# Kernel optimization log

Measured on AMD Instinct MI355X. Metric: run time of the kernel, lower is better.

## Reference

```python
import jax, jax.numpy as jnp
import numpy as np

NUM_HEADS = 16
LN_EPS = 1e-5


def _transpose_qkv(X, num_heads):
    # Faithful to the repo's (buggy) transpose_qkv:
    # (B,S,D) -> (B,S,H,D/H) -> permute (B,H,S,D/H) -> reshape (B,S,D)
    B, S, D = X.shape
    X = X.reshape(B, S, num_heads, D // num_heads)
    X = jnp.transpose(X, (0, 2, 1, 3))
    return X.reshape(B, S, D)


def _layer_norm(x, w, b):
    mu = jnp.mean(x, axis=-1, keepdims=True)
    var = jnp.var(x, axis=-1, keepdims=True)
    return (x - mu) * jax.lax.rsqrt(var + LN_EPS) * w + b


def setup_inputs() -> dict:
    key = jax.random.key(0)
    ks = jax.random.split(key, 4)
    B, S, D = 4, 2048, 1024
    scale = 1.0 / np.sqrt(D)
    return {
        "src": jax.random.normal(ks[0], (B, S, D), dtype=jnp.float32),
        "W_q": jax.random.normal(ks[1], (D, D), dtype=jnp.float32) * scale,
        "W_k": jax.random.normal(ks[2], (D, D), dtype=jnp.float32) * scale,
        "W_v": jax.random.normal(ks[3], (D, D), dtype=jnp.float32) * scale,
        "ln1_w": jnp.ones((D,), dtype=jnp.float32),
        "ln1_b": jnp.zeros((D,), dtype=jnp.float32),
        "ln2_w": jnp.ones((D,), dtype=jnp.float32),
        "ln2_b": jnp.zeros((D,), dtype=jnp.float32),
    }


def reference(src, W_q, W_k, W_v, ln1_w, ln1_b, ln2_w, ln2_b):
    # W_* stored as (in, out): y = x @ W  (equivalent to torch Linear, bias=False)
    q = _transpose_qkv(src @ W_q, NUM_HEADS)  # (B,S,D)
    k = _transpose_qkv(src @ W_k, NUM_HEADS)
    v = _transpose_qkv(src @ W_v, NUM_HEADS)
    d = q.shape[-1]  # note: full hidden dim, per the buggy transpose_qkv
    scores = jnp.einsum("bqd,bkd->bqk", q, k) / jnp.sqrt(jnp.float32(d))
    a = jax.nn.softmax(scores, axis=-1)          # (B,S,S) attention weights
    att = jnp.einsum("bqk,bkd->bqd", a, v)       # (B,S,D)
    src2 = _layer_norm(att, ln1_w, ln1_b)        # norm1
    X = _layer_norm(src + src2, ln2_w, ln2_b)    # AddNorm (dropout=0 in eval)
    return (X, a)
```

## Files before the change

### kernel.cpp

```cpp
#include <hip/hip_runtime.h>

typedef _Float16 f16;
typedef __attribute__((ext_vector_type(2))) _Float16 f16x2;
typedef __attribute__((ext_vector_type(4))) _Float16 f16x4;
typedef __attribute__((ext_vector_type(8))) _Float16 f16x8;
typedef __attribute__((ext_vector_type(4))) float f32x4;

#define D_MODEL 1024
#define SEQ 2048
#define NBATCH 4
#define NROWS (NBATCH * SEQ)

__device__ __forceinline__ void gload16(const void* g, void* l) {
  __builtin_amdgcn_global_load_lds(
      (__attribute__((address_space(1))) void*)(void*)g,
      (__attribute__((address_space(3))) void*)l, 16, 0, 0);
}

#define BARF                                   \
  do {                                         \
    asm volatile("" ::: "memory");             \
    __builtin_amdgcn_s_barrier();              \
    asm volatile("" ::: "memory");             \
  } while (0)
#define LGK asm volatile("s_waitcnt lgkmcnt(0)" ::: "memory")
#define PRIO1 __builtin_amdgcn_s_setprio(1)
#define PRIO0 __builtin_amdgcn_s_setprio(0)


#define STAGE_A(D, H)                                        \
  {                                                          \
    f16* d_ = lds + ((D) * 2 + (H)) * 8192 + t * 8;          \
    gload16((H) ? aP2 : aP0, d_);                            \
    gload16((H) ? aP3 : aP1, d_ + 4096);                     \
  }
#define STAGE_B(D, H)                                        \
  {                                                          \
    if constexpr (BN == 256) {                               \
      f16* d_ = lds + 32768 + ((D) * 2 + (H)) * 8192 + t * 8;\
      gload16((H) ? bP2 : bP0, d_);                          \
      gload16((H) ? bP3 : bP1, d_ + 4096);                   \
    } else {                                                 \
      f16* d_ = lds + 32768 + (D) * 8192 + t * 8;            \
      gload16(bP0, d_);                                      \
      gload16(bP1, d_ + 4096);                               \
    }                                                        \
  }
#define ADVA                                                 \
  {                                                          \
    if (ka < NT - 1) {                                       \
      ka++;                                                  \
      aP0 += stepA; aP1 += stepA; aP2 += stepA; aP3 += stepA;\
    }                                                        \
  }
#define ADVB                                                 \
  {                                                          \
    if (kb < NT - 1) {                                       \
      kb++;                                                  \
      bP0 += stepB; bP1 += stepB;                            \
      if constexpr (BN == 256) { bP2 += stepB; bP3 += stepB; } \
    }                                                        \
  }
#define VMC_STEADY                                           \
  {                                                          \
    if constexpr (BN == 256) {                               \
      asm volatile("s_waitcnt vmcnt(4)" ::: "memory");       \
    } else {                                                 \
      asm volatile("s_waitcnt vmcnt(2)" ::: "memory");       \
    }                                                        \
  }
#define RD_A(D, MH)                                          \
  _Pragma("unroll") for (int mi = 0; mi < 4; ++mi)           \
  _Pragma("unroll") for (int kh = 0; kh < 2; ++kh) {         \
    const int rr = (MH) * 64 + mi * 16 + fr;                 \
    fa[mi][kh] = *(const f16x8*)(lds + ((D) * 2 + wm) * 8192 \
        + rr * 64 + (((g0 + kh * 4) ^ (rr & 7)) << 3));      \
  }
#define RD_B(D, NH)                                          \
  _Pragma("unroll") for (int j = 0; j < NJ; ++j)             \
  _Pragma("unroll") for (int kh = 0; kh < 2; ++kh) {         \
    int rbr, base;                                           \
    if constexpr (BN == 256) {                               \
      rbr = (wn & 1) * 64 + fr * 4 + (NH) * 2 + j;           \
      base = 32768 + ((D) * 2 + (wn >> 1)) * 8192;           \
    } else {                                                 \
      rbr = wn * 32 + fr * 2 + (NH);                         \
      base = 32768 + (D) * 8192;                             \
    }                                                        \
    fb[NH][j][kh] = *(const f16x8*)(lds + base + rbr * 64 +  \
        (((g0 + kh * 4) ^ ((rbr >> 2) & 7)) << 3));          \
  }
#define MFMA_Q(MH, NH)                                       \
  _Pragma("unroll") for (int mi = 0; mi < 4; ++mi)           \
  _Pragma("unroll") for (int j = 0; j < NJ; ++j)             \
  _Pragma("unroll") for (int kh = 0; kh < 2; ++kh)           \
    acc[((MH) * 4 + mi) * 2 * NJ + (NH) * NJ + j] =          \
        __builtin_amdgcn_mfma_f32_16x16x32_f16(              \
            fa[mi][kh], fb[NH][j][kh],                       \
            acc[((MH) * 4 + mi) * 2 * NJ + (NH) * NJ + j], 0, 0, 0);

template <int BN>
__device__ __forceinline__ void gemm8p(
    const f16* aP0, const f16* aP1, const f16* aP2, const f16* aP3,
    const f16* bP0, const f16* bP1, const f16* bP2, const f16* bP3,
    int stepA, int stepB, int NT, f16* lds, f32x4* acc)
{
  constexpr int NJ = BN / 128;
  const int t = threadIdx.x, l = t & 63;
  const int w = t >> 6, wm = w >> 2, wn = w & 3;
  const int fr = l & 15, g0 = l >> 4;
  f16x8 fa[4][2], fb[2][NJ][2];
#pragma unroll
  for (int i = 0; i < 8 * 2 * NJ; ++i) acc[i] = f32x4{0.f, 0.f, 0.f, 0.f};
  int ka = 0, kb = 0;
  (void)bP2; (void)bP3;

  STAGE_A(0, 0); STAGE_A(0, 1); ADVA;
  if constexpr (BN == 256) { STAGE_B(0, 0); STAGE_B(0, 1); }
  else { STAGE_B(0, 0); }
  ADVB;
  if constexpr (BN == 256) { STAGE_B(1, 0); STAGE_B(1, 1); }
  else { STAGE_B(1, 0); }
  ADVB;
  VMC_STEADY;
  BARF;

#pragma unroll 1
  for (int it = 0; it < NT / 2; ++it) {
    RD_A(0, 0); RD_B(0, 0);
    STAGE_A(1, 0);
    BARF; LGK;
    PRIO1; MFMA_Q(0, 0); PRIO0;
    BARF;
    RD_B(0, 1);
    STAGE_A(1, 1); ADVA;
    BARF; LGK;
    PRIO1; MFMA_Q(0, 1); PRIO0;
    BARF;
    RD_A(0, 1);
    STAGE_B(0, 0);
    if constexpr (BN == 128) ADVB;
    BARF; LGK;
    PRIO1; MFMA_Q(1, 0); PRIO0;
    BARF;
    if constexpr (BN == 256) { STAGE_B(0, 1); ADVB; }
    VMC_STEADY;
    BARF;
    PRIO1; MFMA_Q(1, 1); PRIO0;
    BARF;
    RD_A(1, 0); RD_B(1, 0);
    STAGE_A(0, 0);
    BARF; LGK;
    PRIO1; MFMA_Q(0, 0); PRIO0;
    BARF;
    RD_B(1, 1);
    STAGE_A(0, 1); ADVA;
    BARF; LGK;
    PRIO1; MFMA_Q(0, 1); PRIO0;
    BARF;
    RD_A(1, 1);
    STAGE_B(1, 0);
    if constexpr (BN == 128) ADVB;
    BARF; LGK;
    PRIO1; MFMA_Q(1, 0); PRIO0;
    BARF;
    if constexpr (BN == 256) { STAGE_B(1, 1); ADVB; }
    VMC_STEADY;
    BARF;
    PRIO1; MFMA_Q(1, 1); PRIO0;
    BARF;
  }
}

__global__ __launch_bounds__(512, 2) void k_qkv3(
    const f16* __restrict__ srch, const f16* __restrict__ wt,
    f16* __restrict__ qp, f16* __restrict__ kp, f16* __restrict__ vp)
{
  __shared__ f16 lds[49152];
  const int t = threadIdx.x, l = t & 63;
  const int w = t >> 6, wm = w >> 2, wn = w & 3;
  const int fr = l & 15, g0 = l >> 4, c = t & 7;
  const int z = blockIdx.y >> 3, cb = blockIdx.y & 7;
  const f16 *aP[4], *bP[2];
#pragma unroll
  for (int i = 0; i < 4; ++i) {
    const int rl = i * 64 + (t >> 3);
    aP[i] = srch + (size_t)(blockIdx.x * 256 + rl) * 1024 + ((c ^ (rl & 7)) << 3);
  }
#pragma unroll
  for (int i = 0; i < 2; ++i) {
    const int rl = i * 64 + (t >> 3);
    bP[i] = wt + ((size_t)z << 20) + (size_t)(cb * 128 + rl) * 1024 +
            ((c ^ ((rl >> 2) & 7)) << 3);
  }
  f32x4 acc[16];
  gemm8p<128>(aP[0], aP[1], aP[2], aP[3], bP[0], bP[1], bP[0], bP[0],
              64, 64, 16, lds, acc);
  f16* dst = (z == 0) ? qp : (z == 1 ? kp : vp);
  const int col = cb * 128 + wn * 32 + fr * 2;
#pragma unroll
  for (int mi = 0; mi < 8; ++mi)
#pragma unroll
    for (int q = 0; q < 4; ++q) {
      const int row = blockIdx.x * 256 + wm * 128 + mi * 16 + g0 * 4 + q;
      f16x2 o = {(f16)acc[mi * 2 + 0][q], (f16)acc[mi * 2 + 1][q]};
      *(f16x2*)(dst + (size_t)row * 1024 + col) = o;
    }
}

__global__ __launch_bounds__(512, 2) void k_scores(
    const f16* __restrict__ qp, const f16* __restrict__ kp,
    f16* __restrict__ abf)
{
  __shared__ f16 lds[65536];
  const int t = threadIdx.x, l = t & 63;
  const int w = t >> 6, wm = w >> 2, wn = w & 3;
  const int fr = l & 15, g0 = l >> 4, c = t & 7;
  const int b = blockIdx.z;
  const f16* qb = qp + ((size_t)b << 21);
  const f16* kb = kp + ((size_t)b << 21);
  const f16 *aP[4], *bP[4];
#pragma unroll
  for (int i = 0; i < 4; ++i) {
    const int rl = i * 64 + (t >> 3);
    const int spA = blockIdx.x * 256 + rl;
    aP[i] = qb + (size_t)((spA & 127) << 4) * 1024 + ((spA >> 7) << 6) +
            ((c ^ (rl & 7)) << 3);
    const int spB = blockIdx.y * 256 + rl;
    bP[i] = kb + (size_t)((spB & 127) << 4) * 1024 + ((spB >> 7) << 6) +
            ((c ^ ((rl >> 2) & 7)) << 3);
  }
  f32x4 acc[32];
  gemm8p<256>(aP[0], aP[1], aP[2], aP[3], bP[0], bP[1], bP[2], bP[3],
              1024, 1024, 16, lds, acc);
  f16* Cb = abf + ((size_t)b << 22);
  const int col = blockIdx.y * 256 + wn * 64 + fr * 4;
#pragma unroll
  for (int mi = 0; mi < 8; ++mi)
#pragma unroll
    for (int q = 0; q < 4; ++q) {
      const int row = blockIdx.x * 256 + wm * 128 + mi * 16 + g0 * 4 + q;
      f16x4 o = {(f16)(acc[mi * 4 + 0][q] * 0.03125f),
                 (f16)(acc[mi * 4 + 1][q] * 0.03125f),
                 (f16)(acc[mi * 4 + 2][q] * 0.03125f),
                 (f16)(acc[mi * 4 + 3][q] * 0.03125f)};
      *(f16x4*)(Cb + (size_t)row * 2048 + col) = o;
    }
}

__global__ __launch_bounds__(512, 2) void k_att(
    const f16* __restrict__ abf, const f16* __restrict__ vtT,
    f16* __restrict__ attb)
{
  __shared__ f16 lds[49152];
  const int t = threadIdx.x, l = t & 63;
  const int w = t >> 6, wm = w >> 2, wn = w & 3;
  const int fr = l & 15, g0 = l >> 4, c = t & 7;
  const int b = blockIdx.z;
  const f16* ab = abf + ((size_t)b << 22);
  const f16* vb = vtT + ((size_t)b << 21);
  const f16 *aP[4], *bP[2];
#pragma unroll
  for (int i = 0; i < 4; ++i) {
    const int rl = i * 64 + (t >> 3);
    aP[i] = ab + (size_t)(blockIdx.x * 256 + rl) * 2048 + ((c ^ (rl & 7)) << 3);
  }
#pragma unroll
  for (int i = 0; i < 2; ++i) {
    const int rl = i * 64 + (t >> 3);
    bP[i] = vb + (size_t)(blockIdx.y * 128 + rl) * 2048 +
            ((c ^ ((rl >> 2) & 7)) << 3);
  }
  f32x4 acc[16];
  gemm8p<128>(aP[0], aP[1], aP[2], aP[3], bP[0], bP[1], bP[0], bP[0],
              64, 64, 32, lds, acc);
  f16* Cb = attb + ((size_t)b << 21);
  const int col = blockIdx.y * 128 + wn * 32 + fr * 2;
#pragma unroll
  for (int mi = 0; mi < 8; ++mi)
#pragma unroll
    for (int q = 0; q < 4; ++q) {
      const int row = blockIdx.x * 256 + wm * 128 + mi * 16 + g0 * 4 + q;
      f16x2 o = {(f16)acc[mi * 2 + 0][q], (f16)acc[mi * 2 + 1][q]};
      *(f16x2*)(Cb + (size_t)row * 1024 + col) = o;
    }
}

__global__ __launch_bounds__(256) void k_scrT(const f16* __restrict__ vp,
                                              f16* __restrict__ vtT)
{
  __shared__ f16 tile[64][68];
  const int t = threadIdx.x;
  const int sp0 = blockIdx.x * 64, dp0 = blockIdx.y * 64;
  const int d6 = dp0 >> 6;
  const int jb = (sp0 >> 7) << 6;
  const int sbase = sp0 & 127;
  const f16* src = vp + ((size_t)blockIdx.z << 21);
  f16* dst = vtT + ((size_t)blockIdx.z << 21);
#pragma unroll
  for (int p = 0; p < 2; ++p) {
    const int u = p * 32 + (t >> 3);
    const int s = ((sbase + u) << 4) | d6;
    const int c = (t & 7) << 3;
    f16x8 v = *(const f16x8*)(src + (size_t)s * 1024 + jb + c);
    *(f16x4*)&tile[u][c]     = f16x4{v[0], v[1], v[2], v[3]};
    *(f16x4*)&tile[u][c + 4] = f16x4{v[4], v[5], v[6], v[7]};
  }
  __syncthreads();
#pragma unroll
  for (int p = 0; p < 2; ++p) {
    const int cc = p * 32 + (t >> 3);
    const int v0 = (t & 7) << 3;
    f16x8 o;
#pragma unroll
    for (int j = 0; j < 8; ++j) o[j] = tile[v0 + j][cc];
    *(f16x8*)(dst + (size_t)(dp0 + cc) * 2048 + sp0 + v0) = o;
  }
}

__global__ __launch_bounds__(256) void k_cast_f16(const float* __restrict__ in,
                                                  f16* __restrict__ out)
{
  const size_t i = (size_t)blockIdx.x * 256 + threadIdx.x;
  const float4* p = (const float4*)in;
  float4 v0 = p[2 * i], v1 = p[2 * i + 1];
  f16x8 o;
  o[0] = (f16)v0.x; o[1] = (f16)v0.y; o[2] = (f16)v0.z; o[3] = (f16)v0.w;
  o[4] = (f16)v1.x; o[5] = (f16)v1.y; o[6] = (f16)v1.z; o[7] = (f16)v1.w;
  *(f16x8*)(out + 8 * i) = o;
}

__global__ __launch_bounds__(256) void k_castT(
    const float* __restrict__ w0, const float* __restrict__ w1,
    const float* __restrict__ w2, f16* __restrict__ out)
{
  const float* in = (blockIdx.z == 0) ? w0 : (blockIdx.z == 1 ? w1 : w2);
  f16* o = out + ((size_t)blockIdx.z << 20);
  __shared__ f16 tile[64][65];
  const int t = threadIdx.x;
  const int rr = t >> 4, c4 = (t & 15) * 4;
  const int r0 = blockIdx.x * 64, c0 = blockIdx.y * 64;
#pragma unroll
  for (int i = 0; i < 4; ++i) {
    float4 f = *(const float4*)(in + (size_t)(r0 + rr + 16 * i) * 1024 + c0 + c4);
    tile[rr + 16 * i][c4 + 0] = (f16)f.x;
    tile[rr + 16 * i][c4 + 1] = (f16)f.y;
    tile[rr + 16 * i][c4 + 2] = (f16)f.z;
    tile[rr + 16 * i][c4 + 3] = (f16)f.w;
  }
  __syncthreads();
#pragma unroll
  for (int i = 0; i < 4; ++i) {
    const int n = c0 + rr + 16 * i;
    f16* dst = o + (size_t)n * 1024 + r0 + c4;
    dst[0] = tile[c4 + 0][rr + 16 * i];
    dst[1] = tile[c4 + 1][rr + 16 * i];
    dst[2] = tile[c4 + 2][rr + 16 * i];
    dst[3] = tile[c4 + 3][rr + 16 * i];
  }
}

__global__ __launch_bounds__(256) void k_softmax(float* __restrict__ out,
                                                 f16* __restrict__ abf)
{
  const size_t base = (size_t)blockIdx.x * 2048;
  const int t = threadIdx.x, lane = t & 63, w = t >> 6;
  f16x8 v = *(const f16x8*)(abf + base + (size_t)t * 8);
  float x[8];
#pragma unroll
  for (int j = 0; j < 8; ++j) x[j] = (float)v[j];
  float m = fmaxf(fmaxf(fmaxf(x[0], x[1]), fmaxf(x[2], x[3])),
                  fmaxf(fmaxf(x[4], x[5]), fmaxf(x[6], x[7])));
#pragma unroll
  for (int off = 1; off < 64; off <<= 1) m = fmaxf(m, __shfl_xor(m, off));
  __shared__ float red[8];
  if (lane == 0) red[w] = m;
  __syncthreads();
  m = fmaxf(fmaxf(red[0], red[1]), fmaxf(red[2], red[3]));
  float s = 0.f;
#pragma unroll
  for (int j = 0; j < 8; ++j) { x[j] = __expf(x[j] - m); s += x[j]; }
#pragma unroll
  for (int off = 1; off < 64; off <<= 1) s += __shfl_xor(s, off);
  if (lane == 0) red[4 + w] = s;
  __syncthreads();
  s = red[4] + red[5] + red[6] + red[7];
  const float inv = 1.0f / s;
#pragma unroll
  for (int j = 0; j < 8; ++j) x[j] *= inv;
  float4 o0 = {x[0], x[1], x[2], x[3]}, o1 = {x[4], x[5], x[6], x[7]};
  ((float4*)(out + base))[2 * t] = o0;
  ((float4*)(out + base))[2 * t + 1] = o1;
  f16x8 ov;
#pragma unroll
  for (int j = 0; j < 8; ++j) ov[j] = (f16)x[j];
  *(f16x8*)(abf + base + (size_t)t * 8) = ov;
}

__global__ __launch_bounds__(256) void k_ln(
    const f16* __restrict__ attb, const float* __restrict__ src,
    const float* __restrict__ w1, const float* __restrict__ b1,
    const float* __restrict__ w2, const float* __restrict__ b2,
    float* __restrict__ out)
{
  const size_t base = (size_t)blockIdx.x * 1024;
  const int t = threadIdx.x, lane = t & 63, w = t >> 6;
  f16x4 a4 = ((const f16x4*)(attb + base))[t];
  float ax = (float)a4[0], ay = (float)a4[1], az = (float)a4[2], aw = (float)a4[3];
  float s = ax + ay + az + aw;
  float s2 = ax * ax + ay * ay + az * az + aw * aw;
#pragma unroll
  for (int off = 1; off < 64; off <<= 1) {
    s += __shfl_xor(s, off);
    s2 += __shfl_xor(s2, off);
  }
  __shared__ float red[16];
  if (lane == 0) { red[w] = s; red[4 + w] = s2; }
  __syncthreads();
  s = red[0] + red[1] + red[2] + red[3];
  s2 = red[4] + red[5] + red[6] + red[7];
  float mu = s * (1.0f / 1024.0f);
  float var = s2 * (1.0f / 1024.0f) - mu * mu;
  float rs = rsqrtf(var + 1e-5f);
  float4 W1 = ((const float4*)w1)[t], B1 = ((const float4*)b1)[t];
  float4 sv = ((const float4*)(src + base))[t];
  float y0 = sv.x + (ax - mu) * rs * W1.x + B1.x;
  float y1 = sv.y + (ay - mu) * rs * W1.y + B1.y;
  float y2 = sv.z + (az - mu) * rs * W1.z + B1.z;
  float y3 = sv.w + (aw - mu) * rs * W1.w + B1.w;
  s = y0 + y1 + y2 + y3;
  s2 = y0 * y0 + y1 * y1 + y2 * y2 + y3 * y3;
#pragma unroll
  for (int off = 1; off < 64; off <<= 1) {
    s += __shfl_xor(s, off);
    s2 += __shfl_xor(s2, off);
  }
  if (lane == 0) { red[8 + w] = s; red[12 + w] = s2; }
  __syncthreads();
  s = red[8] + red[9] + red[10] + red[11];
  s2 = red[12] + red[13] + red[14] + red[15];
  mu = s * (1.0f / 1024.0f);
  var = s2 * (1.0f / 1024.0f) - mu * mu;
  rs = rsqrtf(var + 1e-5f);
  float4 W2 = ((const float4*)w2)[t], B2 = ((const float4*)b2)[t];
  float4 o;
  o.x = (y0 - mu) * rs * W2.x + B2.x;
  o.y = (y1 - mu) * rs * W2.y + B2.y;
  o.z = (y2 - mu) * rs * W2.z + B2.z;
  o.w = (y3 - mu) * rs * W2.w + B2.w;
  ((float4*)(out + base))[t] = o;
}

extern "C" void kernel_launch(void* const* d_in, const int* in_sizes, int n_in,
                              void* d_out, int out_size, void* d_ws, size_t ws_size,
                              hipStream_t stream) {
  const float* src = (const float*)d_in[0];
  const float* Wq  = (const float*)d_in[1];
  const float* Wk  = (const float*)d_in[2];
  const float* Wv  = (const float*)d_in[3];
  const float* l1w = (const float*)d_in[4];
  const float* l1b = (const float*)d_in[5];
  const float* l2w = (const float*)d_in[6];
  const float* l2b = (const float*)d_in[7];
  float* Xout = (float*)d_out;
  float* Aout = Xout + (size_t)NROWS * D_MODEL;

  char* ws = (char*)d_ws;
  f16* srch = (f16*)ws;
  f16* wt   = (f16*)(ws + (16u << 20));
  f16* qp   = (f16*)(ws + (22u << 20));
  f16* kp   = (f16*)(ws + (38u << 20));
  f16* vp   = (f16*)(ws + (54u << 20));
  f16* vtT  = (f16*)(ws + (70u << 20));
  f16* abf  = (f16*)(ws + (86u << 20));
  f16* attb = (f16*)(ws + (118u << 20));

  k_cast_f16<<<4096, 256, 0, stream>>>(src, srch);
  k_castT<<<dim3(16, 16, 3), 256, 0, stream>>>(Wq, Wk, Wv, wt);
  k_qkv3<<<dim3(32, 24), 512, 0, stream>>>(srch, wt, qp, kp, vp);
  k_scrT<<<dim3(32, 16, 4), 256, 0, stream>>>(vp, vtT);
  k_scores<<<dim3(8, 8, 4), 512, 0, stream>>>(qp, kp, abf);
  k_softmax<<<NROWS, 256, 0, stream>>>(Aout, abf);
  k_att<<<dim3(8, 8, 4), 512, 0, stream>>>(abf, vtT, attb);
  k_ln<<<NROWS, 256, 0, stream>>>(attb, src, l1w, l1b, l2w, l2b, Xout);
}
```

Measured before the change: 199.8 us.

## Merge prep and transpose kernels, widen QKV GEMM tile, add partial LDS wait

Fuses the src cast and weight transpose-cast into one launch, and moves the V transpose into the softmax launch as extra blocks. This removes two kernel launches and lets independent work share a grid. The QKV projection now uses 256x256 tiles with a swizzled 1D block order, intended to improve operand reuse and L2 locality. A partial lgkmcnt wait is also inserted in the GEMM main loop. The larger tile doubles the accumulator registers and LDS use, which may reduce occupancy.

New measurement: 201.2 us. About the same (+0.7%).

```diff
diff --git a/kernel.cpp b/kernel.cpp
--- a/kernel.cpp
+++ b/kernel.cpp
@@ -24,6 +24,7 @@
     asm volatile("" ::: "memory");             \
   } while (0)
 #define LGK asm volatile("s_waitcnt lgkmcnt(0)" ::: "memory")
+#define LGK8 asm volatile("s_waitcnt lgkmcnt(8)" ::: "memory")
 #define PRIO1 __builtin_amdgcn_s_setprio(1)
 #define PRIO0 __builtin_amdgcn_s_setprio(0)
 
@@ -129,6 +130,7 @@
   for (int it = 0; it < NT / 2; ++it) {
     RD_A(0, 0); RD_B(0, 0);
     STAGE_A(1, 0);
+    LGK8;
     BARF; LGK;
     PRIO1; MFMA_Q(0, 0); PRIO0;
     BARF;
@@ -150,6 +152,7 @@
     BARF;
     RD_A(1, 0); RD_B(1, 0);
     STAGE_A(0, 0);
+    LGK8;
     BARF; LGK;
     PRIO1; MFMA_Q(0, 0); PRIO0;
     BARF;
@@ -176,35 +179,35 @@
     const f16* __restrict__ srch, const f16* __restrict__ wt,
     f16* __restrict__ qp, f16* __restrict__ kp, f16* __restrict__ vp)
 {
-  __shared__ f16 lds[49152];
+  __shared__ f16 lds[65536];
   const int t = threadIdx.x, l = t & 63;
   const int w = t >> 6, wm = w >> 2, wn = w & 3;
   const int fr = l & 15, g0 = l >> 4, c = t & 7;
-  const int z = blockIdx.y >> 3, cb = blockIdx.y & 7;
-  const f16 *aP[4], *bP[2];
+  const int bid = blockIdx.x;
+  const int sb = (bid & 7) * 48 + (bid >> 3);
+  const int bx = sb & 31, by = sb >> 5;
+  const int z = by >> 2, cb = by & 3;
+  const f16 *aP[4], *bP[4];
 #pragma unroll
   for (int i = 0; i < 4; ++i) {
     const int rl = i * 64 + (t >> 3);
-    aP[i] = srch + (size_t)(blockIdx.x * 256 + rl) * 1024 + ((c ^ (rl & 7)) << 3);
-  }
-#pragma unroll
-  for (int i = 0; i < 2; ++i) {
-    const int rl = i * 64 + (t >> 3);
-    bP[i] = wt + ((size_t)z << 20) + (size_t)(cb * 128 + rl) * 1024 +
+    aP[i] = srch + (size_t)(bx * 256 + rl) * 1024 + ((c ^ (rl & 7)) << 3);
+    bP[i] = wt + ((size_t)z << 20) + (size_t)(cb * 256 + rl) * 1024 +
             ((c ^ ((rl >> 2) & 7)) << 3);
   }
-  f32x4 acc[16];
-  gemm8p<128>(aP[0], aP[1], aP[2], aP[3], bP[0], bP[1], bP[0], bP[0],
+  f32x4 acc[32];
+  gemm8p<256>(aP[0], aP[1], aP[2], aP[3], bP[0], bP[1], bP[2], bP[3],
               64, 64, 16, lds, acc);
   f16* dst = (z == 0) ? qp : (z == 1 ? kp : vp);
-  const int col = cb * 128 + wn * 32 + fr * 2;
+  const int col = cb * 256 + wn * 64 + fr * 4;
 #pragma unroll
   for (int mi = 0; mi < 8; ++mi)
 #pragma unroll
     for (int q = 0; q < 4; ++q) {
-      const int row = blockIdx.x * 256 + wm * 128 + mi * 16 + g0 * 4 + q;
-      f16x2 o = {(f16)acc[mi * 2 + 0][q], (f16)acc[mi * 2 + 1][q]};
-      *(f16x2*)(dst + (size_t)row * 1024 + col) = o;
+      const int row = bx * 256 + wm * 128 + mi * 16 + g0 * 4 + q;
+      f16x4 o = {(f16)acc[mi * 4 + 0][q], (f16)acc[mi * 4 + 1][q],
+                 (f16)acc[mi * 4 + 2][q], (f16)acc[mi * 4 + 3][q]};
+      *(f16x4*)(dst + (size_t)row * 1024 + col) = o;
     }
 }
 
@@ -286,60 +289,30 @@
     }
 }
 
-__global__ __launch_bounds__(256) void k_scrT(const f16* __restrict__ vp,
-                                              f16* __restrict__ vtT)
-{
-  __shared__ f16 tile[64][68];
-  const int t = threadIdx.x;
-  const int sp0 = blockIdx.x * 64, dp0 = blockIdx.y * 64;
-  const int d6 = dp0 >> 6;
-  const int jb = (sp0 >> 7) << 6;
-  const int sbase = sp0 & 127;
-  const f16* src = vp + ((size_t)blockIdx.z << 21);
-  f16* dst = vtT + ((size_t)blockIdx.z << 21);
-#pragma unroll
-  for (int p = 0; p < 2; ++p) {
-    const int u = p * 32 + (t >> 3);
-    const int s = ((sbase + u) << 4) | d6;
-    const int c = (t & 7) << 3;
-    f16x8 v = *(const f16x8*)(src + (size_t)s * 1024 + jb + c);
-    *(f16x4*)&tile[u][c]     = f16x4{v[0], v[1], v[2], v[3]};
-    *(f16x4*)&tile[u][c + 4] = f16x4{v[4], v[5], v[6], v[7]};
-  }
-  __syncthreads();
-#pragma unroll
-  for (int p = 0; p < 2; ++p) {
-    const int cc = p * 32 + (t >> 3);
-    const int v0 = (t & 7) << 3;
+__global__ __launch_bounds__(256) void k_prep(
+    const float* __restrict__ src, const float* __restrict__ w0,
+    const float* __restrict__ w1, const float* __restrict__ w2,
+    f16* __restrict__ srch, f16* __restrict__ wt)
+{
+  const int b = blockIdx.x, t = threadIdx.x;
+  if (b < 4096) {
+    const size_t i = (size_t)b * 256 + t;
+    const float4* p = (const float4*)src;
+    float4 v0 = p[2 * i], v1 = p[2 * i + 1];
     f16x8 o;
-#pragma unroll
-    for (int j = 0; j < 8; ++j) o[j] = tile[v0 + j][cc];
-    *(f16x8*)(dst + (size_t)(dp0 + cc) * 2048 + sp0 + v0) = o;
-  }
-}
-
-__global__ __launch_bounds__(256) void k_cast_f16(const float* __restrict__ in,
-                                                  f16* __restrict__ out)
-{
-  const size_t i = (size_t)blockIdx.x * 256 + threadIdx.x;
-  const float4* p = (const float4*)in;
-  float4 v0 = p[2 * i], v1 = p[2 * i + 1];
-  f16x8 o;
-  o[0] = (f16)v0.x; o[1] = (f16)v0.y; o[2] = (f16)v0.z; o[3] = (f16)v0.w;
-  o[4] = (f16)v1.x; o[5] = (f16)v1.y; o[6] = (f16)v1.z; o[7] = (f16)v1.w;
-  *(f16x8*)(out + 8 * i) = o;
-}
-
-__global__ __launch_bounds__(256) void k_castT(
-    const float* __restrict__ w0, const float* __restrict__ w1,
-    const float* __restrict__ w2, f16* __restrict__ out)
-{
-  const float* in = (blockIdx.z == 0) ? w0 : (blockIdx.z == 1 ? w1 : w2);
-  f16* o = out + ((size_t)blockIdx.z << 20);
+    o[0] = (f16)v0.x; o[1] = (f16)v0.y; o[2] = (f16)v0.z; o[3] = (f16)v0.w;
+    o[4] = (f16)v1.x; o[5] = (f16)v1.y; o[6] = (f16)v1.z; o[7] = (f16)v1.w;
+    *(f16x8*)(srch + 8 * i) = o;
+    return;
+  }
+  const int id = b - 4096;
+  const int z = id >> 8, rem = id & 255;
+  const int bx = rem & 15, by = rem >> 4;
+  const float* in = (z == 0) ? w0 : (z == 1 ? w1 : w2);
+  f16* o = wt + ((size_t)z << 20);
   __shared__ f16 tile[64][65];
-  const int t = threadIdx.x;
   const int rr = t >> 4, c4 = (t & 15) * 4;
-  const int r0 = blockIdx.x * 64, c0 = blockIdx.y * 64;
+  const int r0 = bx * 64, c0 = by * 64;
 #pragma unroll
   for (int i = 0; i < 4; ++i) {
     float4 f = *(const float4*)(in + (size_t)(r0 + rr + 16 * i) * 1024 + c0 + c4);
@@ -360,41 +333,74 @@
   }
 }
 
-__global__ __launch_bounds__(256) void k_softmax(float* __restrict__ out,
-                                                 f16* __restrict__ abf)
-{
-  const size_t base = (size_t)blockIdx.x * 2048;
-  const int t = threadIdx.x, lane = t & 63, w = t >> 6;
-  f16x8 v = *(const f16x8*)(abf + base + (size_t)t * 8);
-  float x[8];
-#pragma unroll
-  for (int j = 0; j < 8; ++j) x[j] = (float)v[j];
-  float m = fmaxf(fmaxf(fmaxf(x[0], x[1]), fmaxf(x[2], x[3])),
-                  fmaxf(fmaxf(x[4], x[5]), fmaxf(x[6], x[7])));
-#pragma unroll
-  for (int off = 1; off < 64; off <<= 1) m = fmaxf(m, __shfl_xor(m, off));
-  __shared__ float red[8];
-  if (lane == 0) red[w] = m;
+__global__ __launch_bounds__(256) void k_softscr(
+    float* __restrict__ out, f16* __restrict__ abf,
+    const f16* __restrict__ vp, f16* __restrict__ vtT)
+{
+  __shared__ f16 shm[64][68];
+  const int t = threadIdx.x;
+  if (blockIdx.x < 8192) {
+    float* red = (float*)&shm[0][0];
+    const size_t base = (size_t)blockIdx.x * 2048;
+    const int lane = t & 63, w = t >> 6;
+    f16x8 v = *(const f16x8*)(abf + base + (size_t)t * 8);
+    float x[8];
+#pragma unroll
+    for (int j = 0; j < 8; ++j) x[j] = (float)v[j];
+    float m = fmaxf(fmaxf(fmaxf(x[0], x[1]), fmaxf(x[2], x[3])),
+                    fmaxf(fmaxf(x[4], x[5]), fmaxf(x[6], x[7])));
+#pragma unroll
+    for (int off = 1; off < 64; off <<= 1) m = fmaxf(m, __shfl_xor(m, off));
+    if (lane == 0) red[w] = m;
+    __syncthreads();
+    m = fmaxf(fmaxf(red[0], red[1]), fmaxf(red[2], red[3]));
+    float s = 0.f;
+#pragma unroll
+    for (int j = 0; j < 8; ++j) { x[j] = __expf(x[j] - m); s += x[j]; }
+#pragma unroll
+    for (int off = 1; off < 64; off <<= 1) s += __shfl_xor(s, off);
+    if (lane == 0) red[4 + w] = s;
+    __syncthreads();
+    s = red[4] + red[5] + red[6] + red[7];
+    const float inv = 1.0f / s;
+#pragma unroll
+    for (int j = 0; j < 8; ++j) x[j] *= inv;
+    float4 o0 = {x[0], x[1], x[2], x[3]}, o1 = {x[4], x[5], x[6], x[7]};
+    ((float4*)(out + base))[2 * t] = o0;
+    ((float4*)(out + base))[2 * t + 1] = o1;
+    f16x8 ov;
+#pragma unroll
+    for (int j = 0; j < 8; ++j) ov[j] = (f16)x[j];
+    *(f16x8*)(abf + base + (size_t)t * 8) = ov;
+    return;
+  }
+  const int id = blockIdx.x - 8192;
+  const int sx = id & 31, sy = (id >> 5) & 15, bz = id >> 9;
+  const int sp0 = sx * 64, dp0 = sy * 64;
+  const int d6 = dp0 >> 6;
+  const int jb = (sp0 >> 7) << 6;
+  const int sbase = sp0 & 127;
+  const f16* srcv = vp + ((size_t)bz << 21);
+  f16* dstv = vtT + ((size_t)bz << 21);
+#pragma unroll
+  for (int p = 0; p < 2; ++p) {
+    const int u = p * 32 + (t >> 3);
+    const int s = ((sbase + u) << 4) | d6;
+    const int cc = (t & 7) << 3;
+    f16x8 v = *(const f16x8*)(srcv + (size_t)s * 1024 + jb + cc);
+    *(f16x4*)&shm[u][cc]     = f16x4{v[0], v[1], v[2], v[3]};
+    *(f16x4*)&shm[u][cc + 4] = f16x4{v[4], v[5], v[6], v[7]};
+  }
   __syncthreads();
-  m = fmaxf(fmaxf(red[0], red[1]), fmaxf(red[2], red[3]));
-  float s = 0.f;
-#pragma unroll
-  for (int j = 0; j < 8; ++j) { x[j] = __expf(x[j] - m); s += x[j]; }
-#pragma unroll
-  for (int off = 1; off < 64; off <<= 1) s += __shfl_xor(s, off);
-  if (lane == 0) red[4 + w] = s;
-  __syncthreads();
-  s = red[4] + red[5] + red[6] + red[7];
-  const float inv = 1.0f / s;
-#pragma unroll
-  for (int j = 0; j < 8; ++j) x[j] *= inv;
-  float4 o0 = {x[0], x[1], x[2], x[3]}, o1 = {x[4], x[5], x[6], x[7]};
-  ((float4*)(out + base))[2 * t] = o0;
-  ((float4*)(out + base))[2 * t + 1] = o1;
-  f16x8 ov;
-#pragma unroll
-  for (int j = 0; j < 8; ++j) ov[j] = (f16)x[j];
-  *(f16x8*)(abf + base + (size_t)t * 8) = ov;
+#pragma unroll
+  for (int p = 0; p < 2; ++p) {
+    const int cc = p * 32 + (t >> 3);
+    const int v0 = (t & 7) << 3;
+    f16x8 o;
+#pragma unroll
+    for (int j = 0; j < 8; ++j) o[j] = shm[v0 + j][cc];
+    *(f16x8*)(dstv + (size_t)(dp0 + cc) * 2048 + sp0 + v0) = o;
+  }
 }
 
 __global__ __launch_bounds__(256) void k_ln(
@@ -475,12 +481,10 @@
   f16* abf  = (f16*)(ws + (86u << 20));
   f16* attb = (f16*)(ws + (118u << 20));
 
-  k_cast_f16<<<4096, 256, 0, stream>>>(src, srch);
-  k_castT<<<dim3(16, 16, 3), 256, 0, stream>>>(Wq, Wk, Wv, wt);
-  k_qkv3<<<dim3(32, 24), 512, 0, stream>>>(srch, wt, qp, kp, vp);
-  k_scrT<<<dim3(32, 16, 4), 256, 0, stream>>>(vp, vtT);
+  k_prep<<<4864, 256, 0, stream>>>(src, Wq, Wk, Wv, srch, wt);
+  k_qkv3<<<384, 512, 0, stream>>>(srch, wt, qp, kp, vp);
   k_scores<<<dim3(8, 8, 4), 512, 0, stream>>>(qp, kp, abf);
-  k_softmax<<<NROWS, 256, 0, stream>>>(Aout, abf);
+  k_softscr<<<8192 + 2048, 256, 0, stream>>>(Aout, abf, vp, vtT);
   k_att<<<dim3(8, 8, 4), 512, 0, stream>>>(abf, vtT, attb);
   k_ln<<<NROWS, 256, 0, stream>>>(attb, src, l1w, l1b, l2w, l2b, Xout);
 }
```
